# Kernel optimization log

Hardware: AMD Instinct MI355X
Metric: run time of the kernel (lower is better)

Reference implementation:

```python
import jax, jax.numpy as jnp
import numpy as np

N_NODES = 50000


def setup_inputs() -> dict:
    key = jax.random.key(0)
    k1, k2, k3, k4, k5 = jax.random.split(key, 5)
    in_feats, out_feats = 64, 64
    n_edges = 800000
    feature = jax.random.normal(k1, (N_NODES, in_feats), dtype=jnp.float32)
    edge_src = jax.random.randint(k2, (n_edges,), 0, N_NODES, dtype=jnp.int64)
    edge_dst = jax.random.randint(k3, (n_edges,), 0, N_NODES, dtype=jnp.int64)
    # nn.Linear init scale ~ 1/sqrt(in_feats); plain normal is fine for a numeric reference
    W = jax.random.normal(k4, (out_feats, in_feats), dtype=jnp.float32) / jnp.sqrt(jnp.float32(in_feats))
    b = jax.random.normal(k5, (out_feats,), dtype=jnp.float32) * 0.01
    return {"feature": feature, "edge_src": edge_src, "edge_dst": edge_dst, "W": W, "b": b}


def reference(feature, edge_src, edge_dst, W, b):
    # msg = copy_src('h'): gather src features along edges -> [E, F]
    msgs = feature[edge_src]
    # reduce = mean over mailbox: segment-mean by destination node
    agg = jax.ops.segment_sum(msgs, edge_dst, num_segments=N_NODES)  # [N, F]
    cnt = jax.ops.segment_sum(jnp.ones((edge_src.shape[0],), dtype=feature.dtype),
                              edge_dst, num_segments=N_NODES)  # [N]
    mean = agg / jnp.maximum(cnt, 1.0)[:, None]
    # DGL: nodes with no incoming messages keep their original feature 'h'
    h = jnp.where(cnt[:, None] > 0, mean, feature)
    # apply_nodes: ReLU(W h + b) on all nodes
    return jax.nn.relu(h @ W.T + b)
```

## Files before the change

### kernel.cpp

```cpp
#include <hip/hip_runtime.h>


#define F 64
#define CAP 48
#define QW 64
#define EB 2048
#define OVF_MAX 32768

typedef unsigned int uint;
typedef unsigned short ushort;

__device__ __forceinline__ ushort f2bf(float x) {
    uint u = __float_as_uint(x);
    u += 0x7FFFu + ((u >> 16) & 1u);
    return (ushort)(u >> 16);
}

__global__ __launch_bounds__(256) void k_work(const float* __restrict__ feature,
                                              const float* __restrict__ W,
                                              ushort* __restrict__ Ybf,
                                              const int* __restrict__ esrc,
                                              const int* __restrict__ edst,
                                              int* __restrict__ blkBuf,
                                              int* __restrict__ pfxTab,
                                              int* __restrict__ ovfB,
                                              int N, int E, int G, int QP1) {
    __shared__ alignas(16) char smem[28672];
    int tid = threadIdx.x, bid = blockIdx.x;
    if (bid == 0 && tid == 0) ovfB[0] = 0;

    if (bid < G) {
        float* sWt = (float*)smem;
        float* shh = (float*)(smem + 19456);
        for (int i = tid; i < 4096; i += 256) {
            int fo = i >> 6, k = i & 63;
            sWt[k * 76 + fo] = W[i];
        }
        int n0blk = bid * 32;
        for (int i = tid; i < 512; i += 256) {
            int r = i >> 4, c4 = i & 15;
            int n = n0blk + r;
            float4 v = make_float4(0.f, 0.f, 0.f, 0.f);
            if (n < N) v = ((const float4*)feature)[(long)n * 16 + c4];
            *(float4*)&shh[r * 72 + c4 * 4] = v;
        }
        __syncthreads();
        int npair = tid >> 4, foq = tid & 15;
        int r0 = npair * 2, r1 = r0 + 1;
        float a0=0,a1=0,a2=0,a3=0,b0=0,b1=0,b2=0,b3=0;
#pragma unroll 8
        for (int k = 0; k < 64; ++k) {
            float hA = shh[r0 * 72 + k];
            float hB = shh[r1 * 72 + k];
            float4 wv = *(const float4*)&sWt[k * 76 + foq * 4];
            a0 = fmaf(hA, wv.x, a0); a1 = fmaf(hA, wv.y, a1);
            a2 = fmaf(hA, wv.z, a2); a3 = fmaf(hA, wv.w, a3);
            b0 = fmaf(hB, wv.x, b0); b1 = fmaf(hB, wv.y, b1);
            b2 = fmaf(hB, wv.z, b2); b3 = fmaf(hB, wv.w, b3);
        }
        int nA = n0blk + r0, nB = n0blk + r1;
        if (nA < N) ((ushort4*)Ybf)[(long)nA * 16 + foq] =
            make_ushort4(f2bf(a0), f2bf(a1), f2bf(a2), f2bf(a3));
        if (nB < N) ((ushort4*)Ybf)[(long)nB * 16 + foq] =
            make_ushort4(f2bf(b0), f2bf(b1), f2bf(b2), f2bf(b3));
    } else {
        int* cnt   = (int*)smem;
        int* pfx   = (int*)(smem + 4096);
        int* off   = (int*)(smem + 8192);
        int* sc    = (int*)(smem + 12288);
        int* stage = (int*)(smem + 13312);

        int b = bid - G;
        int ebase = b * EB;
        int d[8], s[8];
        int i0 = ebase + tid * 8;
        if (i0 + 7 < E) {
            int4 a  = *(const int4*)(edst + i0);
            int4 b4 = *(const int4*)(edst + i0 + 4);
            d[0]=a.x; d[1]=a.y; d[2]=a.z; d[3]=a.w;
            d[4]=b4.x; d[5]=b4.y; d[6]=b4.z; d[7]=b4.w;
            int4 c4 = *(const int4*)(esrc + i0);
            int4 e4 = *(const int4*)(esrc + i0 + 4);
            s[0]=c4.x; s[1]=c4.y; s[2]=c4.z; s[3]=c4.w;
            s[4]=e4.x; s[5]=e4.y; s[6]=e4.z; s[7]=e4.w;
        } else {
#pragma unroll
            for (int k = 0; k < 8; ++k) {
                int e = i0 + k;
                d[k] = (e < E) ? edst[e] : -1;
                s[k] = (e < E) ? esrc[e] : 0;
            }
        }
        for (int i = tid; i < 1024; i += 256) cnt[i] = 0;
        __syncthreads();
#pragma unroll
        for (int k = 0; k < 8; ++k)
            if (d[k] >= 0) atomicAdd(&cnt[d[k] >> 6], 1);
        __syncthreads();
        int b0i = tid * 4;
        int c0 = cnt[b0i], c1 = cnt[b0i+1], c2 = cnt[b0i+2], c3 = cnt[b0i+3];
        int s4 = c0 + c1 + c2 + c3;
        sc[tid] = s4;
        __syncthreads();
        for (int dd = 1; dd < 256; dd <<= 1) {
            int t = (tid >= dd) ? sc[tid - dd] : 0;
            __syncthreads();
            sc[tid] += t;
            __syncthreads();
        }
        int run = sc[tid] - s4;
        pfx[b0i]   = run; off[b0i]   = run; run += c0;
        pfx[b0i+1] = run; off[b0i+1] = run; run += c1;
        pfx[b0i+2] = run; off[b0i+2] = run; run += c2;
        pfx[b0i+3] = run; off[b0i+3] = run;
        __syncthreads();
#pragma unroll
        for (int k = 0; k < 8; ++k) {
            if (d[k] >= 0) {
                int q = d[k] >> 6;
                int sl = atomicAdd(&off[q], 1);
                stage[sl] = ((d[k] & 63) << 24) | s[k];
            }
        }
        __syncthreads();
        int total = sc[255];
        for (int i = tid; i < total; i += 256)
            blkBuf[ebase + i] = stage[i];
        for (int i = tid; i < QP1; i += 256)
            pfxTab[b * QP1 + i] = pfx[i];
    }
}

__global__ __launch_bounds__(512) void k_bingather(const ushort* __restrict__ Ybf,
                                                   const int* __restrict__ blkBuf,
                                                   const int* __restrict__ pfxTab,
                                                   int* __restrict__ ovfB,
                                                   const float* __restrict__ bias,
                                                   float* __restrict__ out,
                                                   int N, int S, int QP1) {
    __shared__ int dl[QW];
    __shared__ int bl[QW * CAP];
    int tid = threadIdx.x;
    int q   = blockIdx.x;
    for (int i = tid; i < QW; i += 512) dl[i] = 0;
    __syncthreads();
    for (int b = tid; b < S; b += 512) {
        int lo = pfxTab[b * QP1 + q];
        int hi = pfxTab[b * QP1 + q + 1];
        for (int i = lo; i < hi; ++i) {
            int v = blkBuf[b * EB + i];
            int ll = ((uint)v) >> 24;
            int s = v & 0xFFFFFF;
            int r = atomicAdd(&dl[ll], 1);
            if (r < CAP) bl[ll * CAP + r] = s;
            else { int o = atomicAdd(&ovfB[0], 1);
                   if (o < OVF_MAX) { ovfB[2 + 2*o] = q * QW + ll; ovfB[3 + 2*o] = s; } }
        }
    }
    __syncthreads();
    int wv = tid >> 6, lane = tid & 63;
    int g = lane >> 3, c = lane & 7;
    const uint4* Y16 = (const uint4*)Ybf;
    for (int pass = 0; pass < QW / 8; ++pass) {
        int ll = pass * 8 + wv;
        int n = q * QW + ll;
        if (n < N) {
            int d = dl[ll];
            int m = min(d, CAP);
            float acc[2][8];
#pragma unroll
            for (int ch = 0; ch < 2; ++ch)
#pragma unroll
                for (int j = 0; j < 8; ++j) acc[ch][j] = 0.f;
            int last = m - 1;
            for (int base = 0; base < m; base += 16) {
#pragma unroll
                for (int ch = 0; ch < 2; ++ch) {
                    int jdx = base + ch * 8 + g;
                    int s = bl[ll * CAP + min(jdx, last)];
                    uint4 qv = Y16[(long)s * 8 + c];
                    if (jdx < m) {
                        acc[ch][0] += __uint_as_float(qv.x << 16);
                        acc[ch][1] += __uint_as_float(qv.x & 0xFFFF0000u);
                        acc[ch][2] += __uint_as_float(qv.y << 16);
                        acc[ch][3] += __uint_as_float(qv.y & 0xFFFF0000u);
                        acc[ch][4] += __uint_as_float(qv.z << 16);
                        acc[ch][5] += __uint_as_float(qv.z & 0xFFFF0000u);
                        acc[ch][6] += __uint_as_float(qv.w << 16);
                        acc[ch][7] += __uint_as_float(qv.w & 0xFFFF0000u);
                    }
                }
            }
            if (d > CAP) {
                int no = ovfB[0]; if (no > OVF_MAX) no = OVF_MAX;
                if (g == 0) {
                    for (int i = 0; i < no; ++i) {
                        if (ovfB[2 + 2*i] == n) {
                            int s = ovfB[3 + 2*i];
                            uint4 qv = Y16[(long)s * 8 + c];
                            acc[0][0] += __uint_as_float(qv.x << 16);
                            acc[0][1] += __uint_as_float(qv.x & 0xFFFF0000u);
                            acc[0][2] += __uint_as_float(qv.y << 16);
                            acc[0][3] += __uint_as_float(qv.y & 0xFFFF0000u);
                            acc[0][4] += __uint_as_float(qv.z << 16);
                            acc[0][5] += __uint_as_float(qv.z & 0xFFFF0000u);
                            acc[0][6] += __uint_as_float(qv.w << 16);
                            acc[0][7] += __uint_as_float(qv.w & 0xFFFF0000u);
                        }
                    }
                }
            }
#pragma unroll
            for (int j = 0; j < 8; ++j)
                acc[0][j] += acc[1][j];
#pragma unroll
            for (int j = 0; j < 8; ++j) {
                float v = acc[0][j];
                v += __shfl_xor(v, 8);
                v += __shfl_xor(v, 16);
                v += __shfl_xor(v, 32);
                acc[0][j] = v;
            }
            float sel = acc[0][0];
#pragma unroll
            for (int j = 1; j < 8; ++j) sel = (g == j) ? acc[0][j] : sel;
            int fw = c * 8 + g;
            float hv;
            if (d > 0) hv = sel / (float)d;
            else       hv = __uint_as_float(((uint)Ybf[(long)n * F + fw]) << 16);
            out[(long)n * F + fw] = fmaxf(hv + bias[fw], 0.0f);
        }
    }
}

__global__ __launch_bounds__(256) void k_gemm13(const float* __restrict__ feature,
                                                const float* __restrict__ W,
                                                ushort* __restrict__ Ybf, int N,
                                                int* __restrict__ deg, int n4,
                                                int* __restrict__ ovfB) {
    {
        int gt = blockIdx.x * 256 + threadIdx.x;
        if (gt == 0) ovfB[0] = 0;
        for (int i = gt; i < n4; i += gridDim.x * 256)
            ((int4*)deg)[i] = make_int4(0, 0, 0, 0);
    }
    __shared__ float sWt[64 * 76];
    __shared__ float shh[32 * 72];
    int tid = threadIdx.x;
    for (int i = tid; i < 4096; i += 256) {
        int fo = i >> 6, k = i & 63;
        sWt[k * 76 + fo] = W[i];
    }
    int n0blk = blockIdx.x * 32;
    for (int i = tid; i < 512; i += 256) {
        int r = i >> 4, c4 = i & 15;
        int n = n0blk + r;
        float4 v = make_float4(0.f, 0.f, 0.f, 0.f);
        if (n < N) v = ((const float4*)feature)[(long)n * 16 + c4];
        *(float4*)&shh[r * 72 + c4 * 4] = v;
    }
    __syncthreads();
    int npair = tid >> 4, foq = tid & 15;
    int r0 = npair * 2, r1 = r0 + 1;
    float a0=0,a1=0,a2=0,a3=0,b0=0,b1=0,b2=0,b3=0;
#pragma unroll 8
    for (int k = 0; k < 64; ++k) {
        float hA = shh[r0 * 72 + k];
        float hB = shh[r1 * 72 + k];
        float4 wv = *(const float4*)&sWt[k * 76 + foq * 4];
        a0 = fmaf(hA, wv.x, a0); a1 = fmaf(hA, wv.y, a1);
        a2 = fmaf(hA, wv.z, a2); a3 = fmaf(hA, wv.w, a3);
        b0 = fmaf(hB, wv.x, b0); b1 = fmaf(hB, wv.y, b1);
        b2 = fmaf(hB, wv.z, b2); b3 = fmaf(hB, wv.w, b3);
    }
    int nA = n0blk + r0, nB = n0blk + r1;
    if (nA < N) ((ushort4*)Ybf)[(long)nA * 16 + foq] =
        make_ushort4(f2bf(a0), f2bf(a1), f2bf(a2), f2bf(a3));
    if (nB < N) ((ushort4*)Ybf)[(long)nB * 16 + foq] =
        make_ushort4(f2bf(b0), f2bf(b1), f2bf(b2), f2bf(b3));
}

__global__ __launch_bounds__(256) void k_scatter13(const int* __restrict__ esrc,
                                                   const int* __restrict__ edst,
                                                   int* __restrict__ deg,
                                                   int* __restrict__ bucket,
                                                   int* __restrict__ ovfB, int E) {
    int base = (blockIdx.x * 256 + threadIdx.x) * 4;
    if (base + 3 < E) {
        int4 d4 = *(const int4*)(edst + base);
        int4 s4 = *(const int4*)(esrc + base);
        int r0 = atomicAdd(&deg[d4.x], 1);
        int r1 = atomicAdd(&deg[d4.y], 1);
        int r2 = atomicAdd(&deg[d4.z], 1);
        int r3 = atomicAdd(&deg[d4.w], 1);
        if (r0 < CAP) bucket[d4.x * CAP + r0] = s4.x;
        else { int o = atomicAdd(&ovfB[0], 1); if (o < OVF_MAX) { ovfB[2 + 2*o] = d4.x; ovfB[3 + 2*o] = s4.x; } }
        if (r1 < CAP) bucket[d4.y * CAP + r1] = s4.y;
        else { int o = atomicAdd(&ovfB[0], 1); if (o < OVF_MAX) { ovfB[2 + 2*o] = d4.y; ovfB[3 + 2*o] = s4.y; } }
        if (r2 < CAP) bucket[d4.z * CAP + r2] = s4.z;
        else { int o = atomicAdd(&ovfB[0], 1); if (o < OVF_MAX) { ovfB[2 + 2*o] = d4.z; ovfB[3 + 2*o] = s4.z; } }
        if (r3 < CAP) bucket[d4.w * CAP + r3] = s4.w;
        else { int o = atomicAdd(&ovfB[0], 1); if (o < OVF_MAX) { ovfB[2 + 2*o] = d4.w; ovfB[3 + 2*o] = s4.w; } }
    } else {
        for (int e = base; e < E; ++e) {
            int d = edst[e], s = esrc[e];
            int r = atomicAdd(&deg[d], 1);
            if (r < CAP) bucket[d * CAP + r] = s;
            else { int o = atomicAdd(&ovfB[0], 1); if (o < OVF_MAX) { ovfB[2 + 2*o] = d; ovfB[3 + 2*o] = s; } }
        }
    }
}

__global__ __launch_bounds__(256) void k_gatherG(const ushort* __restrict__ Ybf,
                                                 const int* __restrict__ deg,
                                                 const int* __restrict__ bucket,
                                                 const int* __restrict__ ovf,
                                                 const float* __restrict__ bias,
                                                 float* __restrict__ out, int N) {
    int tid = threadIdx.x;
    int w = tid >> 6, lane = tid & 63;
    int g = lane >> 3, c = lane & 7;
    int n = blockIdx.x * 4 + w;
    if (n >= N) return;
    int d = deg[n];
    int m = min(d, CAP);
    int boff = n * CAP;
    const uint4* Y16 = (const uint4*)Ybf;
    float acc[4][8];
#pragma unroll
    for (int ch = 0; ch < 4; ++ch)
#pragma unroll
        for (int j = 0; j < 8; ++j) acc[ch][j] = 0.f;
    int last = m - 1;
    for (int base = 0; base < m; base += 32) {
#pragma unroll
        for (int ch = 0; ch < 4; ++ch) {
            int jdx = base + ch * 8 + g;
            int s = bucket[boff + min(jdx, last)];
            uint4 qv = Y16[(long)s * 8 + c];
            if (jdx < m) {
                acc[ch][0] += __uint_as_float(qv.x << 16);
                acc[ch][1] += __uint_as_float(qv.x & 0xFFFF0000u);
                acc[ch][2] += __uint_as_float(qv.y << 16);
                acc[ch][3] += __uint_as_float(qv.y & 0xFFFF0000u);
                acc[ch][4] += __uint_as_float(qv.z << 16);
                acc[ch][5] += __uint_as_float(qv.z & 0xFFFF0000u);
                acc[ch][6] += __uint_as_float(qv.w << 16);
                acc[ch][7] += __uint_as_float(qv.w & 0xFFFF0000u);
            }
        }
    }
    if (d > CAP) {
        int no = ovf[0]; if (no > OVF_MAX) no = OVF_MAX;
        if (g == 0) {
            for (int i = 0; i < no; ++i) {
                if (ovf[2 + 2*i] == n) {
                    int s = ovf[3 + 2*i];
                    uint4 qv = Y16[(long)s * 8 + c];
                    acc[0][0] += __uint_as_float(qv.x << 16);
                    acc[0][1] += __uint_as_float(qv.x & 0xFFFF0000u);
                    acc[0][2] += __uint_as_float(qv.y << 16);
                    acc[0][3] += __uint_as_float(qv.y & 0xFFFF0000u);
                    acc[0][4] += __uint_as_float(qv.z << 16);
                    acc[0][5] += __uint_as_float(qv.z & 0xFFFF0000u);
                    acc[0][6] += __uint_as_float(qv.w << 16);
                    acc[0][7] += __uint_as_float(qv.w & 0xFFFF0000u);
                }
            }
        }
    }
#pragma unroll
    for (int j = 0; j < 8; ++j)
        acc[0][j] += (acc[1][j] + acc[2][j]) + acc[3][j];
#pragma unroll
    for (int j = 0; j < 8; ++j) {
        float v = acc[0][j];
        v += __shfl_xor(v, 8);
        v += __shfl_xor(v, 16);
        v += __shfl_xor(v, 32);
        acc[0][j] = v;
    }
    float sel = acc[0][0];
#pragma unroll
    for (int j = 1; j < 8; ++j) sel = (g == j) ? acc[0][j] : sel;
    int fw = c * 8 + g;
    float hv;
    if (d > 0) hv = sel / (float)d;
    else       hv = __uint_as_float(((uint)Ybf[(long)n * F + fw]) << 16);
    out[(long)n * F + fw] = fmaxf(hv + bias[fw], 0.0f);
}

__global__ __launch_bounds__(256) void gcn_edge_scatter(const float* __restrict__ feature,
                                                        const int* __restrict__ esrc,
                                                        const int* __restrict__ edst,
                                                        float* __restrict__ agg,
                                                        float* __restrict__ cnt, int E) {
    int t = blockIdx.x * blockDim.x + threadIdx.x;
    int e = t >> 6, f = t & 63;
    if (e >= E) return;
    atomicAdd(&agg[(long)edst[e] * F + f], feature[(long)esrc[e] * F + f]);
    if (f == 0) atomicAdd(&cnt[edst[e]], 1.0f);
}
__global__ __launch_bounds__(256) void gcn_node_apply(const float* __restrict__ feature,
                                                      const float* __restrict__ W,
                                                      const float* __restrict__ bias,
                                                      const float* __restrict__ cnt,
                                                      float* __restrict__ inout, int N) {
    __shared__ float sWt[64 * 65];
    __shared__ float sh[4][64];
    int tid = threadIdx.x;
    for (int i = tid; i < 64 * 64; i += 256) {
        int fo = i >> 6, k = i & 63;
        sWt[k * 65 + fo] = W[i];
    }
    int w = tid >> 6, f = tid & 63;
    int n = blockIdx.x * 4 + w;
    float h = 0.0f;
    if (n < N) {
        float c = cnt[n];
        h = (c > 0.0f) ? inout[(long)n * F + f] / c : feature[(long)n * F + f];
    }
    sh[w][f] = h;
    __syncthreads();
    float acc = bias[f];
#pragma unroll
    for (int k = 0; k < 64; ++k) acc = fmaf(sh[w][k], sWt[k * 65 + f], acc);
    if (n < N) inout[(long)n * F + f] = fmaxf(acc, 0.0f);
}

extern "C" void kernel_launch(void* const* d_in, const int* in_sizes, int n_in,
                              void* d_out, int out_size, void* d_ws, size_t ws_size,
                              hipStream_t stream) {
    const float* feature = (const float*)d_in[0];
    const int*   esrc    = (const int*)d_in[1];
    const int*   edst    = (const int*)d_in[2];
    const float* W       = (const float*)d_in[3];
    const float* bias    = (const float*)d_in[4];

    int N = in_sizes[0] / F;
    int E = in_sizes[1];

    int G   = (N + 31) / 32;
    int S   = (E + EB - 1) / EB;
    int Q   = (N + QW - 1) / QW;
    int QP1 = Q + 1;

    auto align256 = [](size_t x) { return (x + 255) & ~(size_t)255; };
    size_t sz_ovf = align256((2 + 2 * (size_t)OVF_MAX) * sizeof(int));
    size_t sz_Y   = align256((size_t)N * F * sizeof(ushort));
    size_t sz_blk = align256((size_t)S * EB * sizeof(int));
    size_t sz_pfx = align256((size_t)S * QP1 * sizeof(int));
    size_t need_new = sz_ovf + sz_Y + sz_blk + sz_pfx;

    size_t sz_deg    = align256((size_t)N * sizeof(int));
    size_t sz_bucket = align256((size_t)N * CAP * sizeof(int));
    size_t need_mid  = sz_ovf + sz_Y + sz_deg + sz_bucket;

    if (ws_size >= need_new && N <= 65536) {
        char* ws = (char*)d_ws;
        int*    ovfB   = (int*)ws;    ws += sz_ovf;
        ushort* Ybf    = (ushort*)ws; ws += sz_Y;
        int*    blkBuf = (int*)ws;    ws += sz_blk;
        int*    pfxTab = (int*)ws;
        float*  out    = (float*)d_out;

        k_work<<<G + S, 256, 0, stream>>>(feature, W, Ybf, esrc, edst,
                                          blkBuf, pfxTab, ovfB, N, E, G, QP1);
        k_bingather<<<Q, 512, 0, stream>>>(Ybf, blkBuf, pfxTab, ovfB,
                                           bias, out, N, S, QP1);
    } else if (ws_size >= need_mid) {
        char* ws = (char*)d_ws;
        int*    ovfB   = (int*)ws;    ws += sz_ovf;
        ushort* Ybf    = (ushort*)ws; ws += sz_Y;
        int*    deg    = (int*)ws;    ws += sz_deg;
        int*    bucket = (int*)ws;
        float*  out    = (float*)d_out;
        int n4 = (N + 3) / 4;
        int gE4 = (E + 1023) / 1024;

        k_gemm13<<<G, 256, 0, stream>>>(feature, W, Ybf, N, deg, n4, ovfB);
        k_scatter13<<<gE4, 256, 0, stream>>>(esrc, edst, deg, bucket, ovfB, E);
        k_gatherG<<<(N + 3) / 4, 256, 0, stream>>>(Ybf, deg, bucket, ovfB, bias, out, N);
    } else {
        float* agg = (float*)d_out;
        float* cnt = (float*)d_ws;
        hipMemsetAsync(agg, 0, (size_t)N * F * sizeof(float), stream);
        hipMemsetAsync(cnt, 0, (size_t)N * sizeof(float), stream);
        long total = (long)E * F;
        gcn_edge_scatter<<<(int)((total + 255) / 256), 256, 0, stream>>>(
            feature, esrc, edst, agg, cnt, E);
        gcn_node_apply<<<(N + 3) / 4, 256, 0, stream>>>(feature, W, bias, cnt, agg, N);
    }
}
```

Baseline: 53.02 us.

## Retile fused GEMM blocks to 64 nodes with 4x4 register tiles

The GEMM part of the fused work kernel now handles 64 nodes per block instead of 32. Features are stored transposed in shared memory so each thread loads a float4 of four nodes per k, giving a 4x4 register tile per thread instead of 2x4. The goal is to halve the number of GEMM blocks and the redundant per-block W staging, and to raise the FMA-to-LDS ratio. In exchange the kernel needs more shared memory per block, which may lower occupancy for the edge-binning blocks that share this kernel, and the transposed stores to shared memory may cause bank conflicts.

```diff
diff --git a/kernel.cpp b/kernel.cpp
--- a/kernel.cpp
+++ b/kernel.cpp
@@ -25,7 +25,7 @@
                                               int* __restrict__ pfxTab,
                                               int* __restrict__ ovfB,
                                               int N, int E, int G, int QP1) {
-    __shared__ alignas(16) char smem[28672];
+    __shared__ alignas(16) char smem[36864];
     int tid = threadIdx.x, bid = blockIdx.x;
     if (bid == 0 && tid == 0) ovfB[0] = 0;
 
@@ -36,33 +36,42 @@
             int fo = i >> 6, k = i & 63;
             sWt[k * 76 + fo] = W[i];
         }
-        int n0blk = bid * 32;
-        for (int i = tid; i < 512; i += 256) {
-            int r = i >> 4, c4 = i & 15;
-            int n = n0blk + r;
+        int n0blk = bid * 64;
+        for (int i = tid; i < 1024; i += 256) {
+            int nl = i >> 4, c4 = i & 15;
+            int n = n0blk + nl;
             float4 v = make_float4(0.f, 0.f, 0.f, 0.f);
             if (n < N) v = ((const float4*)feature)[(long)n * 16 + c4];
-            *(float4*)&shh[r * 72 + c4 * 4] = v;
+            shh[(c4 * 4 + 0) * 68 + nl] = v.x;
+            shh[(c4 * 4 + 1) * 68 + nl] = v.y;
+            shh[(c4 * 4 + 2) * 68 + nl] = v.z;
+            shh[(c4 * 4 + 3) * 68 + nl] = v.w;
         }
         __syncthreads();
-        int npair = tid >> 4, foq = tid & 15;
-        int r0 = npair * 2, r1 = r0 + 1;
-        float a0=0,a1=0,a2=0,a3=0,b0=0,b1=0,b2=0,b3=0;
+        int nq = tid >> 4, foq = tid & 15;
+        float4 r0 = make_float4(0.f,0.f,0.f,0.f), r1 = r0, r2 = r0, r3 = r0;
 #pragma unroll 8
         for (int k = 0; k < 64; ++k) {
-            float hA = shh[r0 * 72 + k];
-            float hB = shh[r1 * 72 + k];
+            float4 h  = *(const float4*)&shh[k * 68 + nq * 4];
             float4 wv = *(const float4*)&sWt[k * 76 + foq * 4];
-            a0 = fmaf(hA, wv.x, a0); a1 = fmaf(hA, wv.y, a1);
-            a2 = fmaf(hA, wv.z, a2); a3 = fmaf(hA, wv.w, a3);
-            b0 = fmaf(hB, wv.x, b0); b1 = fmaf(hB, wv.y, b1);
-            b2 = fmaf(hB, wv.z, b2); b3 = fmaf(hB, wv.w, b3);
-        }
-        int nA = n0blk + r0, nB = n0blk + r1;
-        if (nA < N) ((ushort4*)Ybf)[(long)nA * 16 + foq] =
-            make_ushort4(f2bf(a0), f2bf(a1), f2bf(a2), f2bf(a3));
-        if (nB < N) ((ushort4*)Ybf)[(long)nB * 16 + foq] =
-            make_ushort4(f2bf(b0), f2bf(b1), f2bf(b2), f2bf(b3));
+            r0.x = fmaf(h.x, wv.x, r0.x); r0.y = fmaf(h.x, wv.y, r0.y);
+            r0.z = fmaf(h.x, wv.z, r0.z); r0.w = fmaf(h.x, wv.w, r0.w);
+            r1.x = fmaf(h.y, wv.x, r1.x); r1.y = fmaf(h.y, wv.y, r1.y);
+            r1.z = fmaf(h.y, wv.z, r1.z); r1.w = fmaf(h.y, wv.w, r1.w);
+            r2.x = fmaf(h.z, wv.x, r2.x); r2.y = fmaf(h.z, wv.y, r2.y);
+            r2.z = fmaf(h.z, wv.z, r2.z); r2.w = fmaf(h.z, wv.w, r2.w);
+            r3.x = fmaf(h.w, wv.x, r3.x); r3.y = fmaf(h.w, wv.y, r3.y);
+            r3.z = fmaf(h.w, wv.z, r3.z); r3.w = fmaf(h.w, wv.w, r3.w);
+        }
+        int nb = n0blk + nq * 4;
+        if (nb + 0 < N) ((ushort4*)Ybf)[(long)(nb + 0) * 16 + foq] =
+            make_ushort4(f2bf(r0.x), f2bf(r0.y), f2bf(r0.z), f2bf(r0.w));
+        if (nb + 1 < N) ((ushort4*)Ybf)[(long)(nb + 1) * 16 + foq] =
+            make_ushort4(f2bf(r1.x), f2bf(r1.y), f2bf(r1.z), f2bf(r1.w));
+        if (nb + 2 < N) ((ushort4*)Ybf)[(long)(nb + 2) * 16 + foq] =
+            make_ushort4(f2bf(r2.x), f2bf(r2.y), f2bf(r2.z), f2bf(r2.w));
+        if (nb + 3 < N) ((ushort4*)Ybf)[(long)(nb + 3) * 16 + foq] =
+            make_ushort4(f2bf(r3.x), f2bf(r3.y), f2bf(r3.z), f2bf(r3.w));
     } else {
         int* cnt   = (int*)smem;
         int* pfx   = (int*)(smem + 4096);
@@ -440,7 +449,7 @@
     int N = in_sizes[0] / F;
     int E = in_sizes[1];
 
-    int G   = (N + 31) / 32;
+    int G   = (N + 63) / 64;
     int S   = (E + EB - 1) / EB;
     int Q   = (N + QW - 1) / QW;
     int QP1 = Q + 1;
@@ -478,7 +487,7 @@
         int n4 = (N + 3) / 4;
         int gE4 = (E + 1023) / 1024;
 
-        k_gemm13<<<G, 256, 0, stream>>>(feature, W, Ybf, N, deg, n4, ovfB);
+        k_gemm13<<<(N + 31) / 32, 256, 0, stream>>>(feature, W, Ybf, N, deg, n4, ovfB);
         k_scatter13<<<gE4, 256, 0, stream>>>(esrc, edst, deg, bucket, ovfB, E);
         k_gatherG<<<(N + 3) / 4, 256, 0, stream>>>(Ybf, deg, bucket, ovfB, bias, out, N);
     } else {
```

Result: slower. 54.10 us (+2.0%).
